# Performance work log

Measured on AMD Instinct MI355X. Metric: run time of the kernel, lower is better.

## Reference

```python
import math
import jax, jax.numpy as jnp
import numpy as np

N_HEADS = 16


def setup_inputs() -> dict:
    key = jax.random.key(0)
    k1, k2 = jax.random.split(key)
    qkv = jax.random.normal(k1, (2, 3072, 2048), dtype=jnp.float32)
    mask = jax.random.randint(k2, (2, 1, 2048), 0, 2).astype(jnp.bool_)
    return {"qkv": qkv, "mask": mask}


def reference(qkv, mask):
    bs, width, length = qkv.shape
    ch = width // (3 * N_HEADS)
    q, k, v = jnp.split(qkv, 3, axis=1)  # each [bs, H*C, T]
    scale = 1.0 / math.sqrt(math.sqrt(ch))  # applied to both q and k
    q = (q * scale).reshape(bs * N_HEADS, ch, length)
    k = (k * scale).reshape(bs * N_HEADS, ch, length)
    # [B*H, T, T] scores
    weight = jnp.einsum('bct,bcs->bts', q, k)
    # mask: [bs, 1, T] bool, True = valid token
    inv = ~mask[:, 0, :]                      # [bs, T]
    pad = inv[:, None, :] | inv[:, :, None]   # [bs, T, T]
    pad = jnp.broadcast_to(pad[:, None], (bs, N_HEADS, length, length))
    pad = pad.reshape(bs * N_HEADS, length, length)
    weight = jnp.where(pad, jnp.finfo(weight.dtype).min, weight)
    weight = jax.nn.softmax(weight.astype(jnp.float32), axis=-1).astype(qkv.dtype)
    a = jnp.einsum('bts,bcs->bct', weight, v.reshape(bs * N_HEADS, ch, length))
    return a.reshape(bs, N_HEADS * ch, length)
```

## Files before the change

kernel.cpp:

```cpp
#include <hip/hip_runtime.h>
#include <float.h>


typedef __attribute__((ext_vector_type(8))) short bf16x8;
typedef __attribute__((ext_vector_type(4))) float f32x4;

#define TSEQ 2048
#define QT_OFF 0L
#define KF_OFF 4194304L
#define VF_OFF 8388608L

#if __has_builtin(__builtin_amdgcn_exp2f)
#define EXPFN(x) __builtin_amdgcn_exp2f(x)
#define SM_SCALE (0.125f * 1.44269504088896f)
#else
#define EXPFN(x) __expf(x)
#define SM_SCALE 0.125f
#endif

__device__ inline short f2bf(float x) {
    union { float f; unsigned u; } un; un.f = x;
    unsigned r = un.u + 0x7fffu + ((un.u >> 16) & 1u);
    return (short)(r >> 16);
}

__device__ inline unsigned pkbf(float a, float b) {
    unsigned au = __float_as_uint(a) + 0x8000u;
    unsigned bu = __float_as_uint(b) + 0x8000u;
    return __builtin_amdgcn_perm(bu, au, 0x07060302u);
}

__global__ __launch_bounds__(256) void prep_kernel(
    const float* __restrict__ qkv, short* __restrict__ ws)
{
    const int tid = threadIdx.x;
    const int job = blockIdx.x;
    if (job < 2048) {
        __shared__ float Ls[64 * 65];
        const int which = job & 1;
        const int rest  = job >> 1;
        const int bh = rest & 31, tt = rest >> 5;
        const int b = bh >> 4, h = bh & 15;
        const float* src = qkv + (long)b * 6291456 + ((long)(which * 1024 + h * 64)) * TSEQ + tt * 64;
        #pragma unroll
        for (int ch = 0; ch < 4; ++ch) {
            int idx = tid + ch * 256;
            int c = idx >> 4, tch = idx & 15;
            float4 v = *(const float4*)(src + (long)c * TSEQ + tch * 4);
            float* L = &Ls[c * 65 + tch * 4];
            L[0] = v.x; L[1] = v.y; L[2] = v.z; L[3] = v.w;
        }
        __syncthreads();
        if (which == 0) {
            short* dst = ws + QT_OFF + ((long)bh * TSEQ + tt * 64) * 64;
            #pragma unroll
            for (int ch = 0; ch < 2; ++ch) {
                int idx = tid + ch * 256;
                int t = idx >> 3, cch = idx & 7;
                bf16x8 o;
                #pragma unroll
                for (int j = 0; j < 8; ++j)
                    o[j] = f2bf(Ls[(cch * 8 + j) * 65 + t] * SM_SCALE);
                *(bf16x8*)(dst + (long)t * 64 + cch * 8) = o;
            }
        } else {
            short* dst = ws + KF_OFF + (long)(bh * 32 + tt) * 4096;
            #pragma unroll
            for (int ch = 0; ch < 2; ++ch) {
                int u = tid + ch * 256;
                int f = u >> 6, lane = u & 63;
                int q = lane >> 4, l15 = lane & 15;
                int hf = f & 1, ns = f >> 1;
                bf16x8 o;
                #pragma unroll
                for (int j = 0; j < 8; ++j)
                    o[j] = f2bf(Ls[(hf * 32 + q * 8 + j) * 65 + ns * 16 + l15]);
                *(bf16x8*)(dst + f * 512 + lane * 8) = o;
            }
        }
    } else {
        const int v = job - 2048;
        const int head = v >> 5, it = v & 31;
        const int b = head >> 4, h = head & 15;
        short* dst = ws + VF_OFF + (long)(head * 32 + it) * 4096;
        #pragma unroll
        for (int ch = 0; ch < 2; ++ch) {
            int u = tid + ch * 256;
            int f = u >> 6, lane = u & 63;
            int q = lane >> 4, l15 = lane & 15;
            int hf = f & 1, nc = f >> 1;
            const float* src = qkv + (long)b * 6291456
                + ((long)(2048 + h * 64 + nc * 16 + l15)) * TSEQ
                + it * 64 + hf * 32 + q * 8;
            float4 a  = *(const float4*)src;
            float4 c4 = *(const float4*)(src + 4);
            bf16x8 o;
            o[0] = f2bf(a.x);  o[1] = f2bf(a.y);  o[2] = f2bf(a.z);  o[3] = f2bf(a.w);
            o[4] = f2bf(c4.x); o[5] = f2bf(c4.y); o[6] = f2bf(c4.z); o[7] = f2bf(c4.w);
            *(bf16x8*)(dst + f * 512 + lane * 8) = o;
        }
    }
}

__global__ __launch_bounds__(256, 4) void attn_kernel(
    const short* __restrict__ wsp, const int* __restrict__ mask,
    float* __restrict__ out)
{
    __shared__ __align__(16) char smem[24576];
    short* Ps  = (short*)smem;
    float* mbf = (float*)(smem + 16384);
    float* Os  = (float*)smem;
    float* Lc  = (float*)(smem + 20480);

    const int tid  = threadIdx.x;
    const int lane = tid & 63, wid = tid >> 6;
    const int l15  = lane & 15, quad = lane >> 4;
    const int wq   = wid & 1,  wss  = wid >> 1;

    const int blk  = blockIdx.x;
    const int head = blk & 31;
    const int qt   = blk >> 5;
    const int b    = head >> 4, h = head & 15;
    const int t0   = qt * 64;

    const short* QT = wsp + QT_OFF + (long)head * 131072;
    const short* KF = wsp + KF_OFF + (long)head * 131072;
    const short* VF = wsp + VF_OFF + (long)head * 131072;
    const long obase = ((long)b * 1024 + h * 64) * TSEQ;

    for (int i = tid; i < TSEQ; i += 256)
        mbf[i] = (mask[b * TSEQ + i] != 0) ? 0.0f : -1e30f;
    __syncthreads();

    bf16x8 qb[2][2];
    #pragma unroll
    for (int nt = 0; nt < 2; ++nt)
        #pragma unroll
        for (int hf = 0; hf < 2; ++hf)
            qb[nt][hf] = *(const bf16x8*)(QT +
                (long)(t0 + wq * 32 + nt * 16 + l15) * 64 + quad * 8 + hf * 32);
    bool qv[2];
    #pragma unroll
    for (int nt = 0; nt < 2; ++nt)
        qv[nt] = (mbf[t0 + wq * 32 + nt * 16 + l15] != 0.0f);

    float l_s[2] = {0.0f, 0.0f};
    f32x4 Oacc[2][4];
    #pragma unroll
    for (int mt = 0; mt < 2; ++mt)
        #pragma unroll
        for (int nc = 0; nc < 4; ++nc)
            #pragma unroll
            for (int r = 0; r < 4; ++r) Oacc[mt][nc][r] = 0.0f;

    short* Pw = Ps + wid * 2048;
    const short* KL = KF + lane * 8;
    const short* VL = VF + lane * 8;

    for (int i = 0; i < 16; ++i) {
        const int it = wss + i * 2;

        const short* kp = KL + (long)it * 4096;
        bf16x8 kc[8];
        #pragma unroll
        for (int f = 0; f < 8; ++f)
            kc[f] = *(const bf16x8*)(kp + f * 512);

        f32x4 bias[4];
        #pragma unroll
        for (int ns = 0; ns < 4; ++ns)
            bias[ns] = *(const f32x4*)&mbf[it * 64 + ns * 16 + quad * 4];

        f32x4 Sacc[4][2];
        __builtin_amdgcn_s_setprio(1);
        #pragma unroll
        for (int ns = 0; ns < 4; ++ns)
            #pragma unroll
            for (int nt = 0; nt < 2; ++nt) {
                Sacc[ns][nt] = __builtin_amdgcn_mfma_f32_16x16x32_bf16(
                    kc[ns * 2 + 0], qb[nt][0], bias[ns], 0, 0, 0);
                Sacc[ns][nt] = __builtin_amdgcn_mfma_f32_16x16x32_bf16(
                    kc[ns * 2 + 1], qb[nt][1], Sacc[ns][nt], 0, 0, 0);
            }
        __builtin_amdgcn_s_setprio(0);

        #pragma unroll
        for (int nt = 0; nt < 2; ++nt) {
            const int row = nt * 16 + l15;
            const int sw  = (row & 7) ^ ((row & 8) >> 1);
            float ls = 0.0f;
            #pragma unroll
            for (int ns = 0; ns < 4; ++ns) {
                float pv[4];
                #pragma unroll
                for (int r = 0; r < 4; ++r) {
                    float e = EXPFN(Sacc[ns][nt][r]);
                    pv[r] = qv[nt] ? 1.0f : e;
                    ls += pv[r];
                }
                const int cbp = (ns * 2 + (quad >> 1)) ^ sw;
                uint2 pk;
                pk.x = pkbf(pv[0], pv[1]);
                pk.y = pkbf(pv[2], pv[3]);
                *(uint2*)&Pw[row * 64 + cbp * 8 + (quad & 1) * 4] = pk;
            }
            ls += __shfl_xor(ls, 16);
            ls += __shfl_xor(ls, 32);
            l_s[nt] += ls;
        }

        const short* vp = VL + (long)it * 4096;
        bf16x8 vf[8];
        #pragma unroll
        for (int f = 0; f < 8; ++f)
            vf[f] = *(const bf16x8*)(vp + f * 512);

        bf16x8 pa[2][2];
        #pragma unroll
        for (int mt = 0; mt < 2; ++mt) {
            const int row = mt * 16 + l15;
            const int sw  = (row & 7) ^ ((row & 8) >> 1);
            #pragma unroll
            for (int hf = 0; hf < 2; ++hf)
                pa[mt][hf] = *(const bf16x8*)&Pw[row * 64 + ((quad + 4 * hf) ^ sw) * 8];
        }
        __builtin_amdgcn_s_setprio(1);
        #pragma unroll
        for (int hf = 0; hf < 2; ++hf)
            #pragma unroll
            for (int nc = 0; nc < 4; ++nc)
                #pragma unroll
                for (int mt = 0; mt < 2; ++mt)
                    Oacc[mt][nc] = __builtin_amdgcn_mfma_f32_16x16x32_bf16(
                        pa[mt][hf], vf[nc * 2 + hf], Oacc[mt][nc], 0, 0, 0);
        __builtin_amdgcn_s_setprio(0);
    }

    __syncthreads();
    if (quad == 0) {
        Lc[wid * 32 + l15]      = l_s[0];
        Lc[wid * 32 + 16 + l15] = l_s[1];
    }
    __syncthreads();
    float inv[2];
    #pragma unroll
    for (int nt = 0; nt < 2; ++nt)
        inv[nt] = 1.0f / (l_s[nt] + Lc[(wid ^ 2) * 32 + nt * 16 + l15]);
    float iw[2][4];
    #pragma unroll
    for (int mt = 0; mt < 2; ++mt)
        #pragma unroll
        for (int r = 0; r < 4; ++r)
            iw[mt][r] = __shfl(inv[mt], 4 * quad + r);

    if (wss == 0) {
        #pragma unroll
        for (int mt = 0; mt < 2; ++mt)
            #pragma unroll
            for (int nc = 0; nc < 4; ++nc) {
                float4 o;
                o.x = Oacc[mt][nc][0] * iw[mt][0];
                o.y = Oacc[mt][nc][1] * iw[mt][1];
                o.z = Oacc[mt][nc][2] * iw[mt][2];
                o.w = Oacc[mt][nc][3] * iw[mt][3];
                *(float4*)&Os[(nc * 16 + l15) * 68 + wq * 32 + mt * 16 + quad * 4] = o;
            }
    }
    __syncthreads();
    if (wss == 1) {
        #pragma unroll
        for (int mt = 0; mt < 2; ++mt)
            #pragma unroll
            for (int nc = 0; nc < 4; ++nc) {
                float* p = &Os[(nc * 16 + l15) * 68 + wq * 32 + mt * 16 + quad * 4];
                p[0] += Oacc[mt][nc][0] * iw[mt][0];
                p[1] += Oacc[mt][nc][1] * iw[mt][1];
                p[2] += Oacc[mt][nc][2] * iw[mt][2];
                p[3] += Oacc[mt][nc][3] * iw[mt][3];
            }
    }
    __syncthreads();
    #pragma unroll
    for (int ch = 0; ch < 4; ++ch) {
        int idx = tid + ch * 256;
        int c = idx >> 4, tch = idx & 15;
        *(float4*)(out + obase + (long)c * TSEQ + t0 + tch * 4) =
            *(const float4*)&Os[c * 68 + tch * 4];
    }
}

extern "C" void kernel_launch(void* const* d_in, const int* in_sizes, int n_in,
                              void* d_out, int out_size, void* d_ws, size_t ws_size,
                              hipStream_t stream) {
    const float* qkv  = (const float*)d_in[0];
    const int*   mask = (const int*)d_in[1];
    float*       out  = (float*)d_out;
    short*       ws   = (short*)d_ws;
    prep_kernel<<<dim3(3072), dim3(256), 0, stream>>>(qkv, ws);
    attn_kernel<<<dim3(1024), dim3(256), 0, stream>>>(ws, mask, out);
}
```

Before: 137.0 us.

## Split key range four ways per block with 32-query tiles and byte mask flags

Each block now covers 32 queries instead of 64, and its four waves each take a quarter of the key tiles rather than a 2x2 query/key split. This doubles the grid and raises launch bounds to 8 blocks per CU, aiming for better occupancy and latency hiding. The four partial outputs are combined through two shared-memory buffers, and the row-sum normalizer now sums four partials. The float bias fed into the MFMA accumulator is replaced by byte mask flags applied as a select after the exponential, which shrinks shared memory. In exchange, K/V reads from L2 and the per-block mask setup both double.

After: 408.5 us. 2.98x slower.

```diff
diff --git a/kernel.cpp b/kernel.cpp
--- a/kernel.cpp
+++ b/kernel.cpp
@@ -102,26 +102,26 @@
     }
 }
 
-__global__ __launch_bounds__(256, 4) void attn_kernel(
+__global__ __launch_bounds__(256, 8) void attn_kernel(
     const short* __restrict__ wsp, const int* __restrict__ mask,
     float* __restrict__ out)
 {
-    __shared__ __align__(16) char smem[24576];
-    short* Ps  = (short*)smem;
-    float* mbf = (float*)(smem + 16384);
-    float* Os  = (float*)smem;
-    float* Lc  = (float*)(smem + 20480);
+    __shared__ __align__(16) char smem[18944];
+    short* Ps = (short*)smem;
+    unsigned char* mfl = (unsigned char*)(smem + 16384);
+    float* Os0 = (float*)smem;
+    float* Os1 = (float*)(smem + 9216);
+    float* Lc  = (float*)(smem + 18432);
 
     const int tid  = threadIdx.x;
     const int lane = tid & 63, wid = tid >> 6;
     const int l15  = lane & 15, quad = lane >> 4;
-    const int wq   = wid & 1,  wss  = wid >> 1;
 
     const int blk  = blockIdx.x;
     const int head = blk & 31;
     const int qt   = blk >> 5;
     const int b    = head >> 4, h = head & 15;
-    const int t0   = qt * 64;
+    const int t0   = qt * 32;
 
     const short* QT = wsp + QT_OFF + (long)head * 131072;
     const short* KF = wsp + KF_OFF + (long)head * 131072;
@@ -129,7 +129,7 @@
     const long obase = ((long)b * 1024 + h * 64) * TSEQ;
 
     for (int i = tid; i < TSEQ; i += 256)
-        mbf[i] = (mask[b * TSEQ + i] != 0) ? 0.0f : -1e30f;
+        mfl[i] = (mask[b * TSEQ + i] != 0) ? 1 : 0;
     __syncthreads();
 
     bf16x8 qb[2][2];
@@ -138,11 +138,11 @@
         #pragma unroll
         for (int hf = 0; hf < 2; ++hf)
             qb[nt][hf] = *(const bf16x8*)(QT +
-                (long)(t0 + wq * 32 + nt * 16 + l15) * 64 + quad * 8 + hf * 32);
-    bool qv[2];
+                (long)(t0 + nt * 16 + l15) * 64 + quad * 8 + hf * 32);
+    bool qm[2];
     #pragma unroll
     for (int nt = 0; nt < 2; ++nt)
-        qv[nt] = (mbf[t0 + wq * 32 + nt * 16 + l15] != 0.0f);
+        qm[nt] = (mask[b * TSEQ + t0 + nt * 16 + l15] == 0);
 
     float l_s[2] = {0.0f, 0.0f};
     f32x4 Oacc[2][4];
@@ -156,9 +156,10 @@
     short* Pw = Ps + wid * 2048;
     const short* KL = KF + lane * 8;
     const short* VL = VF + lane * 8;
-
-    for (int i = 0; i < 16; ++i) {
-        const int it = wss + i * 2;
+    const f32x4 zc = {0.0f, 0.0f, 0.0f, 0.0f};
+
+    for (int i = 0; i < 8; ++i) {
+        const int it = wid + i * 4;
 
         const short* kp = KL + (long)it * 4096;
         bf16x8 kc[8];
@@ -166,10 +167,10 @@
         for (int f = 0; f < 8; ++f)
             kc[f] = *(const bf16x8*)(kp + f * 512);
 
-        f32x4 bias[4];
+        unsigned fw[4];
         #pragma unroll
         for (int ns = 0; ns < 4; ++ns)
-            bias[ns] = *(const f32x4*)&mbf[it * 64 + ns * 16 + quad * 4];
+            fw[ns] = *(const unsigned*)(mfl + it * 64 + ns * 16 + quad * 4);
 
         f32x4 Sacc[4][2];
         __builtin_amdgcn_s_setprio(1);
@@ -178,7 +179,7 @@
             #pragma unroll
             for (int nt = 0; nt < 2; ++nt) {
                 Sacc[ns][nt] = __builtin_amdgcn_mfma_f32_16x16x32_bf16(
-                    kc[ns * 2 + 0], qb[nt][0], bias[ns], 0, 0, 0);
+                    kc[ns * 2 + 0], qb[nt][0], zc, 0, 0, 0);
                 Sacc[ns][nt] = __builtin_amdgcn_mfma_f32_16x16x32_bf16(
                     kc[ns * 2 + 1], qb[nt][1], Sacc[ns][nt], 0, 0, 0);
             }
@@ -195,7 +196,8 @@
                 #pragma unroll
                 for (int r = 0; r < 4; ++r) {
                     float e = EXPFN(Sacc[ns][nt][r]);
-                    pv[r] = qv[nt] ? 1.0f : e;
+                    float em = ((fw[ns] >> (r * 8)) & 0xffu) ? e : 0.0f;
+                    pv[r] = qm[nt] ? 1.0f : em;
                     ls += pv[r];
                 }
                 const int cbp = (ns * 2 + (quad >> 1)) ^ sw;
@@ -244,8 +246,10 @@
     __syncthreads();
     float inv[2];
     #pragma unroll
-    for (int nt = 0; nt < 2; ++nt)
-        inv[nt] = 1.0f / (l_s[nt] + Lc[(wid ^ 2) * 32 + nt * 16 + l15]);
+    for (int nt = 0; nt < 2; ++nt) {
+        const int off = nt * 16 + l15;
+        inv[nt] = 1.0f / (Lc[off] + Lc[32 + off] + Lc[64 + off] + Lc[96 + off]);
+    }
     float iw[2][4];
     #pragma unroll
     for (int mt = 0; mt < 2; ++mt)
@@ -253,7 +257,8 @@
         for (int r = 0; r < 4; ++r)
             iw[mt][r] = __shfl(inv[mt], 4 * quad + r);
 
-    if (wss == 0) {
+    float* Om = (wid & 1) ? Os1 : Os0;
+    if (wid < 2) {
         #pragma unroll
         for (int mt = 0; mt < 2; ++mt)
             #pragma unroll
@@ -263,16 +268,16 @@
                 o.y = Oacc[mt][nc][1] * iw[mt][1];
                 o.z = Oacc[mt][nc][2] * iw[mt][2];
                 o.w = Oacc[mt][nc][3] * iw[mt][3];
-                *(float4*)&Os[(nc * 16 + l15) * 68 + wq * 32 + mt * 16 + quad * 4] = o;
-            }
-    }
-    __syncthreads();
-    if (wss == 1) {
+                *(float4*)&Om[(nc * 16 + l15) * 36 + mt * 16 + quad * 4] = o;
+            }
+    }
+    __syncthreads();
+    if (wid >= 2) {
         #pragma unroll
         for (int mt = 0; mt < 2; ++mt)
             #pragma unroll
             for (int nc = 0; nc < 4; ++nc) {
-                float* p = &Os[(nc * 16 + l15) * 68 + wq * 32 + mt * 16 + quad * 4];
+                float* p = &Om[(nc * 16 + l15) * 36 + mt * 16 + quad * 4];
                 p[0] += Oacc[mt][nc][0] * iw[mt][0];
                 p[1] += Oacc[mt][nc][1] * iw[mt][1];
                 p[2] += Oacc[mt][nc][2] * iw[mt][2];
@@ -281,11 +286,13 @@
     }
     __syncthreads();
     #pragma unroll
-    for (int ch = 0; ch < 4; ++ch) {
+    for (int ch = 0; ch < 2; ++ch) {
         int idx = tid + ch * 256;
-        int c = idx >> 4, tch = idx & 15;
-        *(float4*)(out + obase + (long)c * TSEQ + t0 + tch * 4) =
-            *(const float4*)&Os[c * 68 + tch * 4];
+        int c = idx >> 3, tch = idx & 7;
+        f32x4 o0 = *(const f32x4*)&Os0[c * 36 + tch * 4];
+        f32x4 o1 = *(const f32x4*)&Os1[c * 36 + tch * 4];
+        f32x4 o = o0 + o1;
+        *(f32x4*)(out + obase + (long)c * TSEQ + t0 + tch * 4) = o;
     }
 }
 
@@ -297,5 +304,5 @@
     float*       out  = (float*)d_out;
     short*       ws   = (short*)d_ws;
     prep_kernel<<<dim3(3072), dim3(256), 0, stream>>>(qkv, ws);
-    attn_kernel<<<dim3(1024), dim3(256), 0, stream>>>(ws, mask, out);
-}
+    attn_kernel<<<dim3(2048), dim3(256), 0, stream>>>(ws, mask, out);
+}
```

## Switch attention to 32x32x16 MFMA with in-register P via permlane32 swap

Applied to the files above, without the earlier changes.

Rewrites the attention inner loop to use 32x32x16 bf16 MFMA tiles instead of 16x16x32, with the prep kernel laying out K and V fragments to match. The softmax probabilities are converted with v_cvt_pk_bf16_f32 and reshuffled into the A-operand layout using v_permlane32_swap, so the LDS round trip for P is gone. This removes LDS writes and reads plus barrier-free shared traffic per iteration and cuts the number of MFMA issues. The cost is larger accumulator register footprint (f32x16) and reliance on gfx950-specific inline asm.

Result: no change. 137.9 us (+0.7%).

```diff
diff --git a/kernel.cpp b/kernel.cpp
--- a/kernel.cpp
+++ b/kernel.cpp
@@ -4,6 +4,7 @@
 
 typedef __attribute__((ext_vector_type(8))) short bf16x8;
 typedef __attribute__((ext_vector_type(4))) float f32x4;
+typedef __attribute__((ext_vector_type(16))) float f32x16;
 
 #define TSEQ 2048
 #define QT_OFF 0L
@@ -24,10 +25,14 @@
     return (short)(r >> 16);
 }
 
-__device__ inline unsigned pkbf(float a, float b) {
-    unsigned au = __float_as_uint(a) + 0x8000u;
-    unsigned bu = __float_as_uint(b) + 0x8000u;
-    return __builtin_amdgcn_perm(bu, au, 0x07060302u);
+__device__ inline unsigned cvtpk(float lo, float hi) {
+    unsigned r;
+    asm("v_cvt_pk_bf16_f32 %0, %1, %2" : "=v"(r) : "v"(lo), "v"(hi));
+    return r;
+}
+
+__device__ inline void pl32swap(unsigned &a, unsigned &b) {
+    asm volatile("v_permlane32_swap_b32 %0, %1" : "+v"(a), "+v"(b));
 }
 
 __global__ __launch_bounds__(256) void prep_kernel(
@@ -35,68 +40,62 @@
 {
     const int tid = threadIdx.x;
     const int job = blockIdx.x;
-    if (job < 2048) {
-        __shared__ float Ls[64 * 65];
-        const int which = job & 1;
-        const int rest  = job >> 1;
-        const int bh = rest & 31, tt = rest >> 5;
-        const int b = bh >> 4, h = bh & 15;
-        const float* src = qkv + (long)b * 6291456 + ((long)(which * 1024 + h * 64)) * TSEQ + tt * 64;
-        #pragma unroll
-        for (int ch = 0; ch < 4; ++ch) {
+    const int tpe  = job >> 10;
+    const int rest = job & 1023;
+    const int bh = rest & 31, tt = rest >> 5;
+    const int b = bh >> 4, h = bh & 15;
+
+    __shared__ float Ls[64 * 65];
+    const float* src = qkv + (long)b * 6291456
+        + ((long)(tpe * 1024 + h * 64)) * TSEQ + tt * 64;
+    #pragma unroll
+    for (int ch = 0; ch < 4; ++ch) {
+        int idx = tid + ch * 256;
+        int c = idx >> 4, tch = idx & 15;
+        float4 v = *(const float4*)(src + (long)c * TSEQ + tch * 4);
+        float* L = &Ls[c * 65 + tch * 4];
+        L[0] = v.x; L[1] = v.y; L[2] = v.z; L[3] = v.w;
+    }
+    __syncthreads();
+
+    if (tpe == 0) {
+        short* dst = ws + QT_OFF + ((long)bh * TSEQ + tt * 64) * 64;
+        #pragma unroll
+        for (int ch = 0; ch < 2; ++ch) {
             int idx = tid + ch * 256;
-            int c = idx >> 4, tch = idx & 15;
-            float4 v = *(const float4*)(src + (long)c * TSEQ + tch * 4);
-            float* L = &Ls[c * 65 + tch * 4];
-            L[0] = v.x; L[1] = v.y; L[2] = v.z; L[3] = v.w;
-        }
-        __syncthreads();
-        if (which == 0) {
-            short* dst = ws + QT_OFF + ((long)bh * TSEQ + tt * 64) * 64;
-            #pragma unroll
-            for (int ch = 0; ch < 2; ++ch) {
-                int idx = tid + ch * 256;
-                int t = idx >> 3, cch = idx & 7;
-                bf16x8 o;
-                #pragma unroll
-                for (int j = 0; j < 8; ++j)
-                    o[j] = f2bf(Ls[(cch * 8 + j) * 65 + t] * SM_SCALE);
-                *(bf16x8*)(dst + (long)t * 64 + cch * 8) = o;
-            }
-        } else {
-            short* dst = ws + KF_OFF + (long)(bh * 32 + tt) * 4096;
-            #pragma unroll
-            for (int ch = 0; ch < 2; ++ch) {
-                int u = tid + ch * 256;
-                int f = u >> 6, lane = u & 63;
-                int q = lane >> 4, l15 = lane & 15;
-                int hf = f & 1, ns = f >> 1;
-                bf16x8 o;
-                #pragma unroll
-                for (int j = 0; j < 8; ++j)
-                    o[j] = f2bf(Ls[(hf * 32 + q * 8 + j) * 65 + ns * 16 + l15]);
-                *(bf16x8*)(dst + f * 512 + lane * 8) = o;
-            }
-        }
-    } else {
-        const int v = job - 2048;
-        const int head = v >> 5, it = v & 31;
-        const int b = head >> 4, h = head & 15;
-        short* dst = ws + VF_OFF + (long)(head * 32 + it) * 4096;
+            int t = idx >> 3, cch = idx & 7;
+            bf16x8 o;
+            #pragma unroll
+            for (int j = 0; j < 8; ++j)
+                o[j] = f2bf(Ls[(cch * 8 + j) * 65 + t] * SM_SCALE);
+            *(bf16x8*)(dst + (long)t * 64 + cch * 8) = o;
+        }
+    } else if (tpe == 1) {
+        short* dst = ws + KF_OFF + (long)(bh * 32 + tt) * 4096;
         #pragma unroll
         for (int ch = 0; ch < 2; ++ch) {
             int u = tid + ch * 256;
             int f = u >> 6, lane = u & 63;
-            int q = lane >> 4, l15 = lane & 15;
-            int hf = f & 1, nc = f >> 1;
-            const float* src = qkv + (long)b * 6291456
-                + ((long)(2048 + h * 64 + nc * 16 + l15)) * TSEQ
-                + it * 64 + hf * 32 + q * 8;
-            float4 a  = *(const float4*)src;
-            float4 c4 = *(const float4*)(src + 4);
+            int st = f >> 2, kk = f & 3;
+            int l31 = lane & 31, H = lane >> 5;
             bf16x8 o;
-            o[0] = f2bf(a.x);  o[1] = f2bf(a.y);  o[2] = f2bf(a.z);  o[3] = f2bf(a.w);
-            o[4] = f2bf(c4.x); o[5] = f2bf(c4.y); o[6] = f2bf(c4.z); o[7] = f2bf(c4.w);
+            #pragma unroll
+            for (int j = 0; j < 8; ++j)
+                o[j] = f2bf(Ls[(kk * 16 + H * 8 + j) * 65 + st * 32 + l31]);
+            *(bf16x8*)(dst + f * 512 + lane * 8) = o;
+        }
+    } else {
+        short* dst = ws + VF_OFF + (long)(bh * 32 + tt) * 4096;
+        #pragma unroll
+        for (int ch = 0; ch < 2; ++ch) {
+            int u = tid + ch * 256;
+            int f = u >> 6, lane = u & 63;
+            int ct = f >> 2, kk = f & 3;
+            int l31 = lane & 31, H = lane >> 5;
+            bf16x8 o;
+            #pragma unroll
+            for (int j = 0; j < 8; ++j)
+                o[j] = f2bf(Ls[(ct * 32 + l31) * 65 + kk * 16 + H * 8 + j]);
             *(bf16x8*)(dst + f * 512 + lane * 8) = o;
         }
     }
@@ -106,178 +105,160 @@
     const short* __restrict__ wsp, const int* __restrict__ mask,
     float* __restrict__ out)
 {
-    __shared__ __align__(16) char smem[24576];
-    short* Ps  = (short*)smem;
-    float* mbf = (float*)(smem + 16384);
+    __shared__ __align__(16) char smem[17920];
+    float* mbf = (float*)smem;
     float* Os  = (float*)smem;
-    float* Lc  = (float*)(smem + 20480);
+    float* Lc  = (float*)(smem + 17408);
 
     const int tid  = threadIdx.x;
     const int lane = tid & 63, wid = tid >> 6;
-    const int l15  = lane & 15, quad = lane >> 4;
-    const int wq   = wid & 1,  wss  = wid >> 1;
+    const int l31  = lane & 31, H = lane >> 5;
+    const int wq   = wid & 1,  wss = wid >> 1;
 
     const int blk  = blockIdx.x;
     const int head = blk & 31;
     const int qt   = blk >> 5;
     const int b    = head >> 4, h = head & 15;
     const int t0   = qt * 64;
+    const int tw   = t0 + wq * 32;
 
     const short* QT = wsp + QT_OFF + (long)head * 131072;
-    const short* KF = wsp + KF_OFF + (long)head * 131072;
-    const short* VF = wsp + VF_OFF + (long)head * 131072;
+    const short* KF = wsp + KF_OFF + (long)head * 131072 + lane * 8;
+    const short* VF = wsp + VF_OFF + (long)head * 131072 + lane * 8;
     const long obase = ((long)b * 1024 + h * 64) * TSEQ;
 
     for (int i = tid; i < TSEQ; i += 256)
         mbf[i] = (mask[b * TSEQ + i] != 0) ? 0.0f : -1e30f;
     __syncthreads();
 
-    bf16x8 qb[2][2];
-    #pragma unroll
-    for (int nt = 0; nt < 2; ++nt)
-        #pragma unroll
-        for (int hf = 0; hf < 2; ++hf)
-            qb[nt][hf] = *(const bf16x8*)(QT +
-                (long)(t0 + wq * 32 + nt * 16 + l15) * 64 + quad * 8 + hf * 32);
-    bool qv[2];
-    #pragma unroll
-    for (int nt = 0; nt < 2; ++nt)
-        qv[nt] = (mbf[t0 + wq * 32 + nt * 16 + l15] != 0.0f);
-
-    float l_s[2] = {0.0f, 0.0f};
-    f32x4 Oacc[2][4];
-    #pragma unroll
-    for (int mt = 0; mt < 2; ++mt)
-        #pragma unroll
-        for (int nc = 0; nc < 4; ++nc)
-            #pragma unroll
-            for (int r = 0; r < 4; ++r) Oacc[mt][nc][r] = 0.0f;
-
-    short* Pw = Ps + wid * 2048;
-    const short* KL = KF + lane * 8;
-    const short* VL = VF + lane * 8;
+    bf16x8 qb[4];
+    #pragma unroll
+    for (int kk = 0; kk < 4; ++kk)
+        qb[kk] = *(const bf16x8*)(QT + (long)(tw + l31) * 64 + kk * 16 + H * 8);
+    const bool qv = (mbf[tw + l31] != 0.0f);
+
+    float l_s = 0.0f;
+    f32x16 Oacc[2];
+    #pragma unroll
+    for (int ct = 0; ct < 2; ++ct)
+        #pragma unroll
+        for (int r = 0; r < 16; ++r) Oacc[ct][r] = 0.0f;
 
     for (int i = 0; i < 16; ++i) {
         const int it = wss + i * 2;
 
-        const short* kp = KL + (long)it * 4096;
+        const short* kp = KF + (long)it * 4096;
         bf16x8 kc[8];
         #pragma unroll
         for (int f = 0; f < 8; ++f)
             kc[f] = *(const bf16x8*)(kp + f * 512);
 
-        f32x4 bias[4];
-        #pragma unroll
-        for (int ns = 0; ns < 4; ++ns)
-            bias[ns] = *(const f32x4*)&mbf[it * 64 + ns * 16 + quad * 4];
-
-        f32x4 Sacc[4][2];
+        f32x16 Sacc[2];
+        #pragma unroll
+        for (int st = 0; st < 2; ++st)
+            #pragma unroll
+            for (int g = 0; g < 4; ++g) {
+                f32x4 b4 = *(const f32x4*)&mbf[it * 64 + st * 32 + g * 8 + H * 4];
+                Sacc[st][4 * g + 0] = b4[0];
+                Sacc[st][4 * g + 1] = b4[1];
+                Sacc[st][4 * g + 2] = b4[2];
+                Sacc[st][4 * g + 3] = b4[3];
+            }
+
         __builtin_amdgcn_s_setprio(1);
         #pragma unroll
-        for (int ns = 0; ns < 4; ++ns)
-            #pragma unroll
-            for (int nt = 0; nt < 2; ++nt) {
-                Sacc[ns][nt] = __builtin_amdgcn_mfma_f32_16x16x32_bf16(
-                    kc[ns * 2 + 0], qb[nt][0], bias[ns], 0, 0, 0);
-                Sacc[ns][nt] = __builtin_amdgcn_mfma_f32_16x16x32_bf16(
-                    kc[ns * 2 + 1], qb[nt][1], Sacc[ns][nt], 0, 0, 0);
-            }
+        for (int st = 0; st < 2; ++st)
+            #pragma unroll
+            for (int kk = 0; kk < 4; ++kk)
+                Sacc[st] = __builtin_amdgcn_mfma_f32_32x32x16_bf16(
+                    kc[st * 4 + kk], qb[kk], Sacc[st], 0, 0, 0);
         __builtin_amdgcn_s_setprio(0);
 
-        #pragma unroll
-        for (int nt = 0; nt < 2; ++nt) {
-            const int row = nt * 16 + l15;
-            const int sw  = (row & 7) ^ ((row & 8) >> 1);
-            float ls = 0.0f;
-            #pragma unroll
-            for (int ns = 0; ns < 4; ++ns) {
-                float pv[4];
-                #pragma unroll
-                for (int r = 0; r < 4; ++r) {
-                    float e = EXPFN(Sacc[ns][nt][r]);
-                    pv[r] = qv[nt] ? 1.0f : e;
-                    ls += pv[r];
-                }
-                const int cbp = (ns * 2 + (quad >> 1)) ^ sw;
-                uint2 pk;
-                pk.x = pkbf(pv[0], pv[1]);
-                pk.y = pkbf(pv[2], pv[3]);
-                *(uint2*)&Pw[row * 64 + cbp * 8 + (quad & 1) * 4] = pk;
-            }
-            ls += __shfl_xor(ls, 16);
-            ls += __shfl_xor(ls, 32);
-            l_s[nt] += ls;
-        }
-
-        const short* vp = VL + (long)it * 4096;
+        const short* vp = VF + (long)it * 4096;
         bf16x8 vf[8];
         #pragma unroll
         for (int f = 0; f < 8; ++f)
             vf[f] = *(const bf16x8*)(vp + f * 512);
 
-        bf16x8 pa[2][2];
-        #pragma unroll
-        for (int mt = 0; mt < 2; ++mt) {
-            const int row = mt * 16 + l15;
-            const int sw  = (row & 7) ^ ((row & 8) >> 1);
-            #pragma unroll
-            for (int hf = 0; hf < 2; ++hf)
-                pa[mt][hf] = *(const bf16x8*)&Pw[row * 64 + ((quad + 4 * hf) ^ sw) * 8];
-        }
+        bf16x8 pa[4];
+        float ls = 0.0f;
+        #pragma unroll
+        for (int st = 0; st < 2; ++st) {
+            #pragma unroll
+            for (int r = 0; r < 16; ++r) {
+                float e = EXPFN(Sacc[st][r]);
+                float pv = qv ? 1.0f : e;
+                ls += pv;
+                Sacc[st][r] = pv;
+            }
+            unsigned w0[4], w1[4];
+            #pragma unroll
+            for (int q = 0; q < 4; ++q) {
+                w0[q] = cvtpk(Sacc[st][4 * q + 0], Sacc[st][4 * q + 1]);
+                w1[q] = cvtpk(Sacc[st][4 * q + 2], Sacc[st][4 * q + 3]);
+            }
+            #pragma unroll
+            for (int kl = 0; kl < 2; ++kl) {
+                unsigned a0 = w0[kl * 2], b0 = w0[kl * 2 + 1];
+                unsigned a1 = w1[kl * 2], b1 = w1[kl * 2 + 1];
+                pl32swap(a0, b0);
+                pl32swap(a1, b1);
+                union { unsigned u[4]; bf16x8 v; } cv;
+                cv.u[0] = a0; cv.u[1] = a1; cv.u[2] = b0; cv.u[3] = b1;
+                pa[st * 2 + kl] = cv.v;
+            }
+        }
+        l_s += ls;
+
         __builtin_amdgcn_s_setprio(1);
         #pragma unroll
-        for (int hf = 0; hf < 2; ++hf)
-            #pragma unroll
-            for (int nc = 0; nc < 4; ++nc)
-                #pragma unroll
-                for (int mt = 0; mt < 2; ++mt)
-                    Oacc[mt][nc] = __builtin_amdgcn_mfma_f32_16x16x32_bf16(
-                        pa[mt][hf], vf[nc * 2 + hf], Oacc[mt][nc], 0, 0, 0);
+        for (int ct = 0; ct < 2; ++ct)
+            #pragma unroll
+            for (int kk = 0; kk < 4; ++kk)
+                Oacc[ct] = __builtin_amdgcn_mfma_f32_32x32x16_bf16(
+                    pa[kk], vf[ct * 4 + kk], Oacc[ct], 0, 0, 0);
         __builtin_amdgcn_s_setprio(0);
     }
 
     __syncthreads();
-    if (quad == 0) {
-        Lc[wid * 32 + l15]      = l_s[0];
-        Lc[wid * 32 + 16 + l15] = l_s[1];
-    }
-    __syncthreads();
-    float inv[2];
-    #pragma unroll
-    for (int nt = 0; nt < 2; ++nt)
-        inv[nt] = 1.0f / (l_s[nt] + Lc[(wid ^ 2) * 32 + nt * 16 + l15]);
-    float iw[2][4];
-    #pragma unroll
-    for (int mt = 0; mt < 2; ++mt)
-        #pragma unroll
-        for (int r = 0; r < 4; ++r)
-            iw[mt][r] = __shfl(inv[mt], 4 * quad + r);
+    l_s += __shfl_xor(l_s, 32);
+    if (lane < 32) Lc[wid * 32 + l31] = l_s;
+    __syncthreads();
+    const float inv = 1.0f / (l_s + Lc[(wid ^ 2) * 32 + l31]);
+    float iw[16];
+    #pragma unroll
+    for (int r = 0; r < 16; ++r)
+        iw[r] = __shfl(inv, (r & 3) + 8 * (r >> 2) + 4 * H);
 
     if (wss == 0) {
         #pragma unroll
-        for (int mt = 0; mt < 2; ++mt)
-            #pragma unroll
-            for (int nc = 0; nc < 4; ++nc) {
+        for (int ct = 0; ct < 2; ++ct) {
+            const int c = ct * 32 + l31;
+            #pragma unroll
+            for (int g = 0; g < 4; ++g) {
                 float4 o;
-                o.x = Oacc[mt][nc][0] * iw[mt][0];
-                o.y = Oacc[mt][nc][1] * iw[mt][1];
-                o.z = Oacc[mt][nc][2] * iw[mt][2];
-                o.w = Oacc[mt][nc][3] * iw[mt][3];
-                *(float4*)&Os[(nc * 16 + l15) * 68 + wq * 32 + mt * 16 + quad * 4] = o;
-            }
+                o.x = Oacc[ct][4 * g + 0] * iw[4 * g + 0];
+                o.y = Oacc[ct][4 * g + 1] * iw[4 * g + 1];
+                o.z = Oacc[ct][4 * g + 2] * iw[4 * g + 2];
+                o.w = Oacc[ct][4 * g + 3] * iw[4 * g + 3];
+                *(float4*)&Os[c * 68 + wq * 32 + g * 8 + H * 4] = o;
+            }
+        }
     }
     __syncthreads();
     if (wss == 1) {
         #pragma unroll
-        for (int mt = 0; mt < 2; ++mt)
-            #pragma unroll
-            for (int nc = 0; nc < 4; ++nc) {
-                float* p = &Os[(nc * 16 + l15) * 68 + wq * 32 + mt * 16 + quad * 4];
-                p[0] += Oacc[mt][nc][0] * iw[mt][0];
-                p[1] += Oacc[mt][nc][1] * iw[mt][1];
-                p[2] += Oacc[mt][nc][2] * iw[mt][2];
-                p[3] += Oacc[mt][nc][3] * iw[mt][3];
-            }
+        for (int ct = 0; ct < 2; ++ct) {
+            const int c = ct * 32 + l31;
+            #pragma unroll
+            for (int g = 0; g < 4; ++g) {
+                float* p = &Os[c * 68 + wq * 32 + g * 8 + H * 4];
+                p[0] += Oacc[ct][4 * g + 0] * iw[4 * g + 0];
+                p[1] += Oacc[ct][4 * g + 1] * iw[4 * g + 1];
+                p[2] += Oacc[ct][4 * g + 2] * iw[4 * g + 2];
+                p[3] += Oacc[ct][4 * g + 3] * iw[4 * g + 3];
+            }
+        }
     }
     __syncthreads();
     #pragma unroll
```
